# Kernel optimization log

Hardware: AMD Instinct MI355X
Metric: run time of the kernel (lower is better)

The kernel has to match this reference:

```python
import jax, jax.numpy as jnp
import numpy as np


def setup_inputs() -> dict:
    key = jax.random.key(0)
    k1, k2, k3 = jax.random.split(key, 3)
    B, H, S, D = 2, 16, 2048, 64
    return {
        "q": jax.random.normal(k1, (B, H, S, D), dtype=jnp.float32),
        "k": jax.random.normal(k2, (B, H, S, D), dtype=jnp.float32),
        "v": jax.random.normal(k3, (B, H, S, D), dtype=jnp.float32),
        "chunk_size": 256,
    }


def reference(q, k, v, chunk_size):
    # Chunked Based linear attention: linear (K^T V) + rank-3 quadratic (K x K x V)
    # inter-chunk state recurrence (shifted/exclusive cumsum over chunks) plus the
    # intra-chunk causal part with kernel  s = q.k;  phi = s + 0.5*s^2.
    B, H, S, D = q.shape
    C = chunk_size
    N = S // C
    scale = D ** (-0.5)

    qc = (q * scale).reshape(B, H, N, C, D)
    kc = k.reshape(B, H, N, C, D)
    vc = v.reshape(B, H, N, C, D)

    # ---- linear inter-chunk state: shifted cumsum of K^T V per chunk ----
    KV = jnp.einsum("bhncd,bhnce->bhnde", kc, vc)            # (B,H,N,D,D)
    S_lin = jnp.cumsum(KV, axis=2) - KV                       # exclusive cumsum
    o_lin = jnp.einsum("bhncd,bhnde->bhnce", qc, S_lin)

    # ---- quadratic inter-chunk state: shifted cumsum of sum_c K_d K_e V_f ----
    KKV = jnp.einsum("bhncd,bhnce,bhncf->bhndef", kc, kc, vc)  # (B,H,N,D,D,D)
    S_quad = jnp.cumsum(KKV, axis=2) - KKV                     # exclusive cumsum
    o_quad = 0.5 * jnp.einsum("bhndef,bhncd,bhnce->bhncf", S_quad, qc, qc)

    # ---- intra-chunk causal quadratic attention ----
    A = jnp.einsum("bhncd,bhnmd->bhncm", qc, kc)               # (B,H,N,C,C)
    mask = jnp.tril(jnp.ones((C, C), dtype=bool))
    Ak = jnp.where(mask, A + 0.5 * A * A, 0.0)
    o_intra = jnp.einsum("bhncm,bhnmf->bhncf", Ak, vc)

    out = (o_lin + o_quad + o_intra).reshape(B, H, S, D)
    return out
```

## Files before the change

### kernel.cpp

```cpp
#include <hip/hip_runtime.h>
#include <stdint.h>

#define SEQ  2048
#define DH   64
#define BH_N 32
#define SCALE 0.125f

typedef __attribute__((ext_vector_type(8))) short short8;
typedef __attribute__((ext_vector_type(4))) short short4b;
typedef __attribute__((ext_vector_type(4))) float f32x4;

static __device__ __forceinline__ unsigned short f2bf(float f) {
  unsigned int u = __float_as_uint(f);
  u += 0x7fffu + ((u >> 16) & 1u);
  return (unsigned short)(u >> 16);
}

typedef __attribute__((address_space(1))) const unsigned char* gp1;
typedef __attribute__((address_space(3))) unsigned char* lp3;
static __device__ __forceinline__ void stage16(const void* g, void* l) {
  __builtin_amdgcn_global_load_lds((gp1)g, (lp3)l, 16, 0, 0);
}

__global__ __launch_bounds__(256) void prep_kernel(
    const float* __restrict__ kin, const float* __restrict__ vin,
    unsigned short* __restrict__ kb, unsigned short* __restrict__ vt2)
{
  const int sb = blockIdx.x;
  const int bh = blockIdx.y;
  const int t  = threadIdx.x;
  const size_t base = ((size_t)bh * SEQ + (size_t)sb * 64) * DH;

  #pragma unroll
  for (int i = 0; i < 4; ++i) {
    int lin = i * 1024 + t * 4;
    float4 f = *reinterpret_cast<const float4*>(kin + base + lin);
    uint2 pk;
    pk.x = (unsigned)f2bf(f.x) | ((unsigned)f2bf(f.y) << 16);
    pk.y = (unsigned)f2bf(f.z) | ((unsigned)f2bf(f.w) << 16);
    *reinterpret_cast<uint2*>(kb + base + lin) = pk;
  }

  #pragma unroll
  for (int uu = 0; uu < 2; ++uu) {
    const int u   = uu * 256 + t;
    const int kgp = u >> 8, ft = (u >> 6) & 3, qd = (u >> 4) & 3, lo = u & 15;
    unsigned short sh[8];
    #pragma unroll
    for (int j = 0; j < 8; ++j) {
      int kg  = kgp * 2 + (j >> 2);
      int key = kg * 16 + qd * 4 + (j & 3);
      sh[j] = f2bf(vin[base + (size_t)key * DH + ft * 16 + lo]);
    }
    uint4 pk;
    pk.x = (unsigned)sh[0] | ((unsigned)sh[1] << 16);
    pk.y = (unsigned)sh[2] | ((unsigned)sh[3] << 16);
    pk.z = (unsigned)sh[4] | ((unsigned)sh[5] << 16);
    pk.w = (unsigned)sh[6] | ((unsigned)sh[7] << 16);
    *reinterpret_cast<uint4*>(vt2 + (((size_t)bh * 32 + sb) * 512 + u) * 8) = pk;
  }
}

__global__ __launch_bounds__(512, 4) void attn_kernel(
    const float* __restrict__ q,
    const unsigned short* __restrict__ kb,
    const unsigned short* __restrict__ vt2,
    float* __restrict__ out)
{
  const int qa   = blockIdx.x;
  const int bh   = blockIdx.y;
  const int tid  = threadIdx.x;
  const int w    = tid >> 6;
  const int lane = tid & 63;
  const int low  = lane & 15;
  const int quad = lane >> 4;
  const int p    = w >> 2;
  const int qsel = (w >> 1) & 1;
  const int rh   = w & 1;

  const int mytile = qsel ? (31 - qa) : qa;
  const int tmax   = 31 - qa;
  const int imax   = tmax >> 1;
  const int r0     = mytile * 64 + rh * 32;

  __shared__ __align__(16) unsigned short kls[2][2][8][512];
  __shared__ __align__(16) unsigned short vls[2][2][512][8];

  const unsigned short* kb_h = kb  + (size_t)bh * SEQ * DH;
  const unsigned short* v2_h = vt2 + (size_t)bh * 32 * 512 * 8;

  short8 aq[2][2];
  #pragma unroll
  for (int h = 0; h < 2; ++h) {
    const float* qp = q + ((size_t)bh * SEQ + r0 + h * 16 + low) * DH + quad * 8;
    #pragma unroll
    for (int ks = 0; ks < 2; ++ks) {
      float4 f0 = *reinterpret_cast<const float4*>(qp + ks * 32);
      float4 f1 = *reinterpret_cast<const float4*>(qp + ks * 32 + 4);
      short8 a;
      a[0] = (short)f2bf(f0.x * SCALE); a[1] = (short)f2bf(f0.y * SCALE);
      a[2] = (short)f2bf(f0.z * SCALE); a[3] = (short)f2bf(f0.w * SCALE);
      a[4] = (short)f2bf(f1.x * SCALE); a[5] = (short)f2bf(f1.y * SCALE);
      a[6] = (short)f2bf(f1.z * SCALE); a[7] = (short)f2bf(f1.w * SCALE);
      aq[h][ks] = a;
    }
  }

  f32x4 oacc[2][4];
  #pragma unroll
  for (int h = 0; h < 2; ++h)
    #pragma unroll
    for (int i = 0; i < 4; ++i) oacc[h][i] = (f32x4){0.f, 0.f, 0.f, 0.f};

  const int cc = w & 3, pp = w >> 2;

  #define STAGE(IP, B)                                                           \
    do {                                                                         \
      const int tile_ = (IP) * 2 + pp;                                           \
      stage16(kb_h + (size_t)(tile_ * 64 + lane) * 64 + cc * 8,                  \
              &kls[B][pp][cc][0]);                                               \
      stage16(kb_h + (size_t)(tile_ * 64 + lane) * 64 + 32 + cc * 8,             \
              &kls[B][pp][cc + 4][0]);                                           \
      stage16(v2_h + (size_t)(tile_ * 512 + cc * 64 + lane) * 8,                 \
              &vls[B][pp][cc * 64][0]);                                          \
      stage16(v2_h + (size_t)(tile_ * 512 + (cc + 4) * 64 + lane) * 8,           \
              &vls[B][pp][(cc + 4) * 64][0]);                                    \
    } while (0)

  STAGE(0, 0);

  for (int i = 0; i <= imax; ++i) {
    const int b = i & 1;
    __builtin_amdgcn_s_barrier();
    if (i < imax) {
      STAGE(i + 1, b ^ 1);
      asm volatile("s_waitcnt vmcnt(4)" ::: "memory");
    } else {
      asm volatile("s_waitcnt vmcnt(0)" ::: "memory");
    }
    __builtin_amdgcn_s_barrier();
    asm volatile("" ::: "memory");

    const int tt = 2 * i + p;
    if (tt > mytile) continue;
    const bool diag = (tt == mytile);

    const unsigned short* kT = &kls[b][p][0][0];
    const unsigned short* vT = &vls[b][p][0][0];

    #pragma unroll
    for (int ntp = 0; ntp < 2; ++ntp) {
      short8 vf[4];
      #pragma unroll
      for (int ft = 0; ft < 4; ++ft)
        vf[ft] = *reinterpret_cast<const short8*>(
            vT + (ntp * 256 + ft * 64 + quad * 16 + low) * 8);

      #pragma unroll
      for (int sub = 0; sub < 2; ++sub) {
        const int nt = ntp * 2 + sub;

        f32x4 s0 = (f32x4){0.f, 0.f, 0.f, 0.f};
        f32x4 s1 = (f32x4){0.f, 0.f, 0.f, 0.f};
        #pragma unroll
        for (int ks = 0; ks < 2; ++ks) {
          short8 kf = *reinterpret_cast<const short8*>(
              kT + (ks * 4 + quad) * 512 + (nt * 16 + low) * 8);
          s0 = __builtin_amdgcn_mfma_f32_16x16x32_bf16(kf, aq[0][ks], s0, 0, 0, 0);
          s1 = __builtin_amdgcn_mfma_f32_16x16x32_bf16(kf, aq[1][ks], s1, 0, 0, 0);
        }

        #pragma unroll
        for (int h = 0; h < 2; ++h) {
          f32x4 s = h ? s1 : s0;
          short4b pf;
          #pragma unroll
          for (int r = 0; r < 4; ++r) {
            float x = s[r];
            float v = __builtin_fmaf(0.5f * x, x, x);
            if (diag && (nt * 16 + quad * 4 + r) > (rh * 32 + h * 16 + low)) v = 0.f;
            pf[r] = (short)f2bf(v);
          }
          #pragma unroll
          for (int ft = 0; ft < 4; ++ft) {
            short4b va = sub
                ? __builtin_shufflevector(vf[ft], vf[ft], 4, 5, 6, 7)
                : __builtin_shufflevector(vf[ft], vf[ft], 0, 1, 2, 3);
            oacc[h][ft] =
                __builtin_amdgcn_mfma_f32_16x16x16bf16_1k(va, pf, oacc[h][ft], 0, 0, 0);
          }
        }
      }
    }
  }

  __syncthreads();
  float* mb = reinterpret_cast<float*>(&kls[0][0][0][0]);
  float* mw = mb + (size_t)(w & 3) * 2048;
  if (p == 1) {
    #pragma unroll
    for (int h = 0; h < 2; ++h)
      #pragma unroll
      for (int ft = 0; ft < 4; ++ft)
        *reinterpret_cast<f32x4*>(&mw[(h * 4 + ft) * 256 + low * 16 + quad * 4]) =
            oacc[h][ft];
  }
  __syncthreads();
  if (p == 0) {
    #pragma unroll
    for (int h = 0; h < 2; ++h) {
      #pragma unroll
      for (int ft = 0; ft < 4; ++ft) {
        f32x4 o = oacc[h][ft];
        f32x4 m = *reinterpret_cast<const f32x4*>(
            &mw[(h * 4 + ft) * 256 + low * 16 + quad * 4]);
        o += m;
        *reinterpret_cast<f32x4*>(
            &out[((size_t)bh * SEQ + r0 + h * 16 + low) * DH + ft * 16 + quad * 4]) = o;
      }
    }
  }
}

extern "C" void kernel_launch(void* const* d_in, const int* in_sizes, int n_in,
                              void* d_out, int out_size, void* d_ws, size_t ws_size,
                              hipStream_t stream)
{
  const float* q = (const float*)d_in[0];
  const float* k = (const float*)d_in[1];
  const float* v = (const float*)d_in[2];
  float* out = (float*)d_out;

  unsigned short* kb  = (unsigned short*)d_ws;
  unsigned short* vt2 = kb + (size_t)BH_N * SEQ * DH;

  prep_kernel<<<dim3(32, BH_N), 256, 0, stream>>>(k, v, kb, vt2);
  attn_kernel<<<dim3(16, BH_N), 512, 0, stream>>>(q, kb, vt2, out);
}
```

Baseline: 144.8 us.

## Process paired query tiles in one 4-wave block with shared K/V staging

The attention kernel drops from 8 waves to 4 waves per block, and each wave now holds both paired query tiles (qa and 31-qa). The block streams the 33 key tiles needed by the pair only once: even and odd steps split across two wave pairs, with each tile routed to the matching accumulator set. The prep kernel goes through LDS so it can write K in a pre-tiled layout with coalesced loads and stores, and bf16 packing switches to a perm-based helper. The aim is to remove duplicated K/V loads and the lopsided work between the two query tiles. The cost is twice as many accumulator and Q registers per wave and fewer waves per block.

```diff
diff --git a/kernel.cpp b/kernel.cpp
--- a/kernel.cpp
+++ b/kernel.cpp
@@ -15,6 +15,11 @@
   u += 0x7fffu + ((u >> 16) & 1u);
   return (unsigned short)(u >> 16);
 }
+static __device__ __forceinline__ unsigned packbf(float a, float b) {
+  unsigned ua = __float_as_uint(a); ua += 0x7fffu + ((ua >> 16) & 1u);
+  unsigned ub = __float_as_uint(b); ub += 0x7fffu + ((ub >> 16) & 1u);
+  return __builtin_amdgcn_perm(ub, ua, 0x07060302);
+}
 
 typedef __attribute__((address_space(1))) const unsigned char* gp1;
 typedef __attribute__((address_space(3))) unsigned char* lp3;
@@ -24,46 +29,54 @@
 
 __global__ __launch_bounds__(256) void prep_kernel(
     const float* __restrict__ kin, const float* __restrict__ vin,
-    unsigned short* __restrict__ kb, unsigned short* __restrict__ vt2)
+    unsigned short* __restrict__ kb2, unsigned short* __restrict__ vt2)
 {
   const int sb = blockIdx.x;
   const int bh = blockIdx.y;
   const int t  = threadIdx.x;
-  const size_t base = ((size_t)bh * SEQ + (size_t)sb * 64) * DH;
+  __shared__ __align__(16) unsigned short lds[4096];
+  const size_t base  = ((size_t)bh * SEQ + (size_t)sb * 64) * DH;
+  const size_t obase = ((size_t)bh * 32 + sb) * 4096;
 
   #pragma unroll
   for (int i = 0; i < 4; ++i) {
-    int lin = i * 1024 + t * 4;
-    float4 f = *reinterpret_cast<const float4*>(kin + base + lin);
-    uint2 pk;
-    pk.x = (unsigned)f2bf(f.x) | ((unsigned)f2bf(f.y) << 16);
-    pk.y = (unsigned)f2bf(f.z) | ((unsigned)f2bf(f.w) << 16);
-    *reinterpret_cast<uint2*>(kb + base + lin) = pk;
-  }
-
+    int idx = i * 256 + t, key = idx >> 4, F = (idx & 15) * 4;
+    float4 f = *reinterpret_cast<const float4*>(kin + base + key * DH + F);
+    int c = (F >> 5) * 4 + ((F >> 3) & 3), jh = (F >> 2) & 1;
+    uint2 pk; pk.x = packbf(f.x, f.y); pk.y = packbf(f.z, f.w);
+    *reinterpret_cast<uint2*>(lds + (c * 64 + key) * 8 + jh * 4) = pk;
+  }
+  __syncthreads();
   #pragma unroll
   for (int uu = 0; uu < 2; ++uu) {
-    const int u   = uu * 256 + t;
-    const int kgp = u >> 8, ft = (u >> 6) & 3, qd = (u >> 4) & 3, lo = u & 15;
-    unsigned short sh[8];
-    #pragma unroll
-    for (int j = 0; j < 8; ++j) {
-      int kg  = kgp * 2 + (j >> 2);
-      int key = kg * 16 + qd * 4 + (j & 3);
-      sh[j] = f2bf(vin[base + (size_t)key * DH + ft * 16 + lo]);
-    }
-    uint4 pk;
-    pk.x = (unsigned)sh[0] | ((unsigned)sh[1] << 16);
-    pk.y = (unsigned)sh[2] | ((unsigned)sh[3] << 16);
-    pk.z = (unsigned)sh[4] | ((unsigned)sh[5] << 16);
-    pk.w = (unsigned)sh[6] | ((unsigned)sh[7] << 16);
-    *reinterpret_cast<uint4*>(vt2 + (((size_t)bh * 32 + sb) * 512 + u) * 8) = pk;
-  }
-}
-
-__global__ __launch_bounds__(512, 4) void attn_kernel(
+    int u = uu * 256 + t;
+    *reinterpret_cast<uint4*>(kb2 + obase + u * 8) =
+        *reinterpret_cast<const uint4*>(lds + u * 8);
+  }
+  __syncthreads();
+  #pragma unroll
+  for (int i = 0; i < 4; ++i) {
+    int idx = i * 256 + t, key = idx >> 4, F = (idx & 15) * 4;
+    float4 f = *reinterpret_cast<const float4*>(vin + base + key * DH + F);
+    int kgp = key >> 5, qd = (key >> 2) & 3, jj = ((key >> 4) & 1) * 4 + (key & 3);
+    int u0 = kgp * 256 + (F >> 4) * 64 + qd * 16 + (F & 15);
+    lds[(u0 + 0) * 8 + jj] = f2bf(f.x);
+    lds[(u0 + 1) * 8 + jj] = f2bf(f.y);
+    lds[(u0 + 2) * 8 + jj] = f2bf(f.z);
+    lds[(u0 + 3) * 8 + jj] = f2bf(f.w);
+  }
+  __syncthreads();
+  #pragma unroll
+  for (int uu = 0; uu < 2; ++uu) {
+    int u = uu * 256 + t;
+    *reinterpret_cast<uint4*>(vt2 + obase + u * 8) =
+        *reinterpret_cast<const uint4*>(lds + u * 8);
+  }
+}
+
+__global__ __launch_bounds__(256, 2) void attn_kernel(
     const float* __restrict__ q,
-    const unsigned short* __restrict__ kb,
+    const unsigned short* __restrict__ kb2,
     const unsigned short* __restrict__ vt2,
     float* __restrict__ out)
 {
@@ -74,150 +87,170 @@
   const int lane = tid & 63;
   const int low  = lane & 15;
   const int quad = lane >> 4;
-  const int p    = w >> 2;
-  const int qsel = (w >> 1) & 1;
+  const int p    = w >> 1;
   const int rh   = w & 1;
-
-  const int mytile = qsel ? (31 - qa) : qa;
-  const int tmax   = 31 - qa;
-  const int imax   = tmax >> 1;
-  const int r0     = mytile * 64 + rh * 32;
-
-  __shared__ __align__(16) unsigned short kls[2][2][8][512];
-  __shared__ __align__(16) unsigned short vls[2][2][512][8];
-
-  const unsigned short* kb_h = kb  + (size_t)bh * SEQ * DH;
-  const unsigned short* v2_h = vt2 + (size_t)bh * 32 * 512 * 8;
-
-  short8 aq[2][2];
-  #pragma unroll
-  for (int h = 0; h < 2; ++h) {
-    const float* qp = q + ((size_t)bh * SEQ + r0 + h * 16 + low) * DH + quad * 8;
-    #pragma unroll
-    for (int ks = 0; ks < 2; ++ks) {
-      float4 f0 = *reinterpret_cast<const float4*>(qp + ks * 32);
-      float4 f1 = *reinterpret_cast<const float4*>(qp + ks * 32 + 4);
-      short8 a;
-      a[0] = (short)f2bf(f0.x * SCALE); a[1] = (short)f2bf(f0.y * SCALE);
-      a[2] = (short)f2bf(f0.z * SCALE); a[3] = (short)f2bf(f0.w * SCALE);
-      a[4] = (short)f2bf(f1.x * SCALE); a[5] = (short)f2bf(f1.y * SCALE);
-      a[6] = (short)f2bf(f1.z * SCALE); a[7] = (short)f2bf(f1.w * SCALE);
-      aq[h][ks] = a;
-    }
-  }
-
-  f32x4 oacc[2][4];
+  const int nB   = 32 - qa;
+
+  __shared__ __align__(16) unsigned short kls[2][2][4096];
+  __shared__ __align__(16) unsigned short vls[2][2][4096];
+
+  const unsigned short* kb_h = kb2 + (size_t)bh * 32 * 4096;
+  const unsigned short* v2_h = vt2 + (size_t)bh * 32 * 4096;
+
+  short8 aqA[2][2], aqB[2][2];
+  #pragma unroll
+  for (int tsel = 0; tsel < 2; ++tsel) {
+    const int qt = tsel ? (31 - qa) : qa;
+    #pragma unroll
+    for (int h = 0; h < 2; ++h) {
+      const float* qp =
+          q + ((size_t)bh * SEQ + qt * 64 + rh * 32 + h * 16 + low) * DH + quad * 8;
+      #pragma unroll
+      for (int ks = 0; ks < 2; ++ks) {
+        float4 f0 = *reinterpret_cast<const float4*>(qp + ks * 32);
+        float4 f1 = *reinterpret_cast<const float4*>(qp + ks * 32 + 4);
+        uint4 uv;
+        uv.x = packbf(f0.x * SCALE, f0.y * SCALE);
+        uv.y = packbf(f0.z * SCALE, f0.w * SCALE);
+        uv.z = packbf(f1.x * SCALE, f1.y * SCALE);
+        uv.w = packbf(f1.z * SCALE, f1.w * SCALE);
+        short8 a = __builtin_bit_cast(short8, uv);
+        if (tsel) aqB[h][ks] = a; else aqA[h][ks] = a;
+      }
+    }
+  }
+
+  f32x4 oaccA[2][4], oaccB[2][4];
   #pragma unroll
   for (int h = 0; h < 2; ++h)
     #pragma unroll
-    for (int i = 0; i < 4; ++i) oacc[h][i] = (f32x4){0.f, 0.f, 0.f, 0.f};
-
-  const int cc = w & 3, pp = w >> 2;
-
-  #define STAGE(IP, B)                                                           \
-    do {                                                                         \
-      const int tile_ = (IP) * 2 + pp;                                           \
-      stage16(kb_h + (size_t)(tile_ * 64 + lane) * 64 + cc * 8,                  \
-              &kls[B][pp][cc][0]);                                               \
-      stage16(kb_h + (size_t)(tile_ * 64 + lane) * 64 + 32 + cc * 8,             \
-              &kls[B][pp][cc + 4][0]);                                           \
-      stage16(v2_h + (size_t)(tile_ * 512 + cc * 64 + lane) * 8,                 \
-              &vls[B][pp][cc * 64][0]);                                          \
-      stage16(v2_h + (size_t)(tile_ * 512 + (cc + 4) * 64 + lane) * 8,           \
-              &vls[B][pp][(cc + 4) * 64][0]);                                    \
+    for (int i = 0; i < 4; ++i) {
+      oaccA[h][i] = (f32x4){0.f, 0.f, 0.f, 0.f};
+      oaccB[h][i] = (f32x4){0.f, 0.f, 0.f, 0.f};
+    }
+
+  const int slot = w & 1;
+  const unsigned short* gsrc = (w >> 1) ? v2_h : kb_h;
+  unsigned short* ldst0 = (w >> 1) ? &vls[0][slot][0] : &kls[0][slot][0];
+  unsigned short* ldst1 = (w >> 1) ? &vls[1][slot][0] : &kls[1][slot][0];
+
+  #define STAGE(I, B)                                                          \
+    do {                                                                       \
+      int s_ = 2 * (I) + slot; if (s_ > 32) s_ = 32;                           \
+      const int T_ = (s_ < nB) ? s_ : (s_ - nB);                               \
+      const unsigned short* gs_ = gsrc + (size_t)T_ * 4096;                    \
+      unsigned short* ld_ = (B) ? ldst1 : ldst0;                               \
+      _Pragma("unroll")                                                        \
+      for (int r_ = 0; r_ < 8; ++r_)                                           \
+        stage16(gs_ + (r_ * 64 + lane) * 8, ld_ + (r_ * 64 + lane) * 8);       \
     } while (0)
 
+  #define COMPUTE(AQ, OACC)                                                    \
+    do {                                                                       \
+      _Pragma("unroll")                                                        \
+      for (int ntp = 0; ntp < 2; ++ntp) {                                      \
+        short8 vf[4];                                                          \
+        _Pragma("unroll")                                                      \
+        for (int ft = 0; ft < 4; ++ft)                                         \
+          vf[ft] = *reinterpret_cast<const short8*>(                           \
+              vT + ((ntp * 4 + ft) * 64 + quad * 16 + low) * 8);               \
+        _Pragma("unroll")                                                      \
+        for (int sub = 0; sub < 2; ++sub) {                                    \
+          const int nt = ntp * 2 + sub;                                        \
+          f32x4 s0 = (f32x4){0.f, 0.f, 0.f, 0.f};                              \
+          f32x4 s1 = (f32x4){0.f, 0.f, 0.f, 0.f};                              \
+          _Pragma("unroll")                                                    \
+          for (int ks = 0; ks < 2; ++ks) {                                     \
+            short8 kf = *reinterpret_cast<const short8*>(                      \
+                kT + ((ks * 4 + quad) * 64 + nt * 16 + low) * 8);              \
+            s0 = __builtin_amdgcn_mfma_f32_16x16x32_bf16(kf, AQ[0][ks], s0, 0, 0, 0); \
+            s1 = __builtin_amdgcn_mfma_f32_16x16x32_bf16(kf, AQ[1][ks], s1, 0, 0, 0); \
+          }                                                                    \
+          _Pragma("unroll")                                                    \
+          for (int h = 0; h < 2; ++h) {                                        \
+            f32x4 sv = h ? s1 : s0;                                            \
+            float pv[4];                                                       \
+            _Pragma("unroll")                                                  \
+            for (int r = 0; r < 4; ++r) {                                      \
+              float x = sv[r];                                                 \
+              pv[r] = __builtin_fmaf(0.5f * x, x, x);                          \
+            }                                                                  \
+            if (diag) {                                                        \
+              _Pragma("unroll")                                                \
+              for (int r = 0; r < 4; ++r)                                      \
+                if ((nt * 16 + quad * 4 + r) > (rh * 32 + h * 16 + low))       \
+                  pv[r] = 0.f;                                                 \
+            }                                                                  \
+            uint2 du; du.x = packbf(pv[0], pv[1]); du.y = packbf(pv[2], pv[3]);\
+            short4b pf = __builtin_bit_cast(short4b, du);                      \
+            _Pragma("unroll")                                                  \
+            for (int ft = 0; ft < 4; ++ft) {                                   \
+              short4b va = sub                                                 \
+                  ? __builtin_shufflevector(vf[ft], vf[ft], 4, 5, 6, 7)        \
+                  : __builtin_shufflevector(vf[ft], vf[ft], 0, 1, 2, 3);       \
+              OACC[h][ft] = __builtin_amdgcn_mfma_f32_16x16x16bf16_1k(         \
+                  va, pf, OACC[h][ft], 0, 0, 0);                               \
+            }                                                                  \
+          }                                                                    \
+        }                                                                      \
+      }                                                                        \
+    } while (0)
+
   STAGE(0, 0);
 
-  for (int i = 0; i <= imax; ++i) {
+  for (int i = 0; i < 17; ++i) {
     const int b = i & 1;
     __builtin_amdgcn_s_barrier();
-    if (i < imax) {
+    if (i < 16) {
       STAGE(i + 1, b ^ 1);
-      asm volatile("s_waitcnt vmcnt(4)" ::: "memory");
+      asm volatile("s_waitcnt vmcnt(8)" ::: "memory");
     } else {
       asm volatile("s_waitcnt vmcnt(0)" ::: "memory");
     }
     __builtin_amdgcn_s_barrier();
     asm volatile("" ::: "memory");
 
-    const int tt = 2 * i + p;
-    if (tt > mytile) continue;
-    const bool diag = (tt == mytile);
-
-    const unsigned short* kT = &kls[b][p][0][0];
-    const unsigned short* vT = &vls[b][p][0][0];
-
-    #pragma unroll
-    for (int ntp = 0; ntp < 2; ++ntp) {
-      short8 vf[4];
-      #pragma unroll
-      for (int ft = 0; ft < 4; ++ft)
-        vf[ft] = *reinterpret_cast<const short8*>(
-            vT + (ntp * 256 + ft * 64 + quad * 16 + low) * 8);
-
-      #pragma unroll
-      for (int sub = 0; sub < 2; ++sub) {
-        const int nt = ntp * 2 + sub;
-
-        f32x4 s0 = (f32x4){0.f, 0.f, 0.f, 0.f};
-        f32x4 s1 = (f32x4){0.f, 0.f, 0.f, 0.f};
-        #pragma unroll
-        for (int ks = 0; ks < 2; ++ks) {
-          short8 kf = *reinterpret_cast<const short8*>(
-              kT + (ks * 4 + quad) * 512 + (nt * 16 + low) * 8);
-          s0 = __builtin_amdgcn_mfma_f32_16x16x32_bf16(kf, aq[0][ks], s0, 0, 0, 0);
-          s1 = __builtin_amdgcn_mfma_f32_16x16x32_bf16(kf, aq[1][ks], s1, 0, 0, 0);
-        }
-
-        #pragma unroll
-        for (int h = 0; h < 2; ++h) {
-          f32x4 s = h ? s1 : s0;
-          short4b pf;
-          #pragma unroll
-          for (int r = 0; r < 4; ++r) {
-            float x = s[r];
-            float v = __builtin_fmaf(0.5f * x, x, x);
-            if (diag && (nt * 16 + quad * 4 + r) > (rh * 32 + h * 16 + low)) v = 0.f;
-            pf[r] = (short)f2bf(v);
-          }
-          #pragma unroll
-          for (int ft = 0; ft < 4; ++ft) {
-            short4b va = sub
-                ? __builtin_shufflevector(vf[ft], vf[ft], 4, 5, 6, 7)
-                : __builtin_shufflevector(vf[ft], vf[ft], 0, 1, 2, 3);
-            oacc[h][ft] =
-                __builtin_amdgcn_mfma_f32_16x16x16bf16_1k(va, pf, oacc[h][ft], 0, 0, 0);
-          }
-        }
-      }
-    }
-  }
-
-  __syncthreads();
-  float* mb = reinterpret_cast<float*>(&kls[0][0][0][0]);
-  float* mw = mb + (size_t)(w & 3) * 2048;
+    const int s = 2 * i + p;
+    if (s > 32) continue;
+    const bool diag = (s == nB - 1) || (s == 32);
+    const unsigned short* kT = &kls[b][p][0];
+    const unsigned short* vT = &vls[b][p][0];
+
+    if (s >= nB) COMPUTE(aqA, oaccA);
+    else         COMPUTE(aqB, oaccB);
+  }
+
+  __syncthreads();
+  float* mb = reinterpret_cast<float*>(&kls[0][0][0]);
+  float* mw = mb + rh * 4096;
   if (p == 1) {
     #pragma unroll
     for (int h = 0; h < 2; ++h)
       #pragma unroll
-      for (int ft = 0; ft < 4; ++ft)
-        *reinterpret_cast<f32x4*>(&mw[(h * 4 + ft) * 256 + low * 16 + quad * 4]) =
-            oacc[h][ft];
+      for (int ft = 0; ft < 4; ++ft) {
+        *reinterpret_cast<f32x4*>(mw + ((0 * 8 + h * 4 + ft) * 256 + lane * 4)) =
+            oaccA[h][ft];
+        *reinterpret_cast<f32x4*>(mw + ((1 * 8 + h * 4 + ft) * 256 + lane * 4)) =
+            oaccB[h][ft];
+      }
   }
   __syncthreads();
   if (p == 0) {
     #pragma unroll
-    for (int h = 0; h < 2; ++h) {
+    for (int tsel = 0; tsel < 2; ++tsel) {
+      const int qt = tsel ? (31 - qa) : qa;
       #pragma unroll
-      for (int ft = 0; ft < 4; ++ft) {
-        f32x4 o = oacc[h][ft];
-        f32x4 m = *reinterpret_cast<const f32x4*>(
-            &mw[(h * 4 + ft) * 256 + low * 16 + quad * 4]);
-        o += m;
-        *reinterpret_cast<f32x4*>(
-            &out[((size_t)bh * SEQ + r0 + h * 16 + low) * DH + ft * 16 + quad * 4]) = o;
-      }
+      for (int h = 0; h < 2; ++h)
+        #pragma unroll
+        for (int ft = 0; ft < 4; ++ft) {
+          f32x4 o = tsel ? oaccB[h][ft] : oaccA[h][ft];
+          f32x4 m = *reinterpret_cast<const f32x4*>(
+              mw + ((tsel * 8 + h * 4 + ft) * 256 + lane * 4));
+          o += m;
+          *reinterpret_cast<f32x4*>(
+              out + ((size_t)bh * SEQ + qt * 64 + rh * 32 + h * 16 + low) * DH +
+              ft * 16 + quad * 4) = o;
+        }
     }
   }
 }
@@ -231,9 +264,9 @@
   const float* v = (const float*)d_in[2];
   float* out = (float*)d_out;
 
-  unsigned short* kb  = (unsigned short*)d_ws;
-  unsigned short* vt2 = kb + (size_t)BH_N * SEQ * DH;
-
-  prep_kernel<<<dim3(32, BH_N), 256, 0, stream>>>(k, v, kb, vt2);
-  attn_kernel<<<dim3(16, BH_N), 512, 0, stream>>>(q, kb, vt2, out);
-}
+  unsigned short* kb2 = (unsigned short*)d_ws;
+  unsigned short* vt2 = kb2 + (size_t)BH_N * SEQ * DH;
+
+  prep_kernel<<<dim3(32, BH_N), 256, 0, stream>>>(k, v, kb2, vt2);
+  attn_kernel<<<dim3(16, BH_N), 256, 0, stream>>>(q, kb2, vt2, out);
+}
```

After: 128.2 us. 11.5% less time.

## Restructure attention into 256-thread blocks with LDS-transposed prep and swizzled grid

Applied to the files above, without the earlier changes.

The prep kernel now transposes K and V through shared memory into the exact per-tile fragment layouts, so loads are coalesced and the LDS staging in the attention kernel becomes contiguous 16-byte copies. The attention kernel drops from 512 to 256 threads per block. Each block now walks every key tile sequentially instead of splitting tiles across two wave groups, which removes the final cross-wave LDS reduction. The grid is flattened with a block-to-head swizzle, and bf16 packing uses a perm-based helper. This trades parallel work per block for higher occupancy and fewer barriers, at the cost of a longer serial loop per block.

```diff
diff --git a/kernel.cpp b/kernel.cpp
--- a/kernel.cpp
+++ b/kernel.cpp
@@ -15,6 +15,11 @@
   u += 0x7fffu + ((u >> 16) & 1u);
   return (unsigned short)(u >> 16);
 }
+static __device__ __forceinline__ unsigned packbf(float a, float b) {
+  unsigned ua = __float_as_uint(a); ua += 0x7fffu + ((ua >> 16) & 1u);
+  unsigned ub = __float_as_uint(b); ub += 0x7fffu + ((ub >> 16) & 1u);
+  return __builtin_amdgcn_perm(ub, ua, 0x07060302);
+}
 
 typedef __attribute__((address_space(1))) const unsigned char* gp1;
 typedef __attribute__((address_space(3))) unsigned char* lp3;
@@ -24,85 +29,91 @@
 
 __global__ __launch_bounds__(256) void prep_kernel(
     const float* __restrict__ kin, const float* __restrict__ vin,
-    unsigned short* __restrict__ kb, unsigned short* __restrict__ vt2)
+    unsigned short* __restrict__ kb2, unsigned short* __restrict__ vt2)
 {
   const int sb = blockIdx.x;
   const int bh = blockIdx.y;
   const int t  = threadIdx.x;
-  const size_t base = ((size_t)bh * SEQ + (size_t)sb * 64) * DH;
+  __shared__ __align__(16) unsigned short lds[4096];
+  const size_t base  = ((size_t)bh * SEQ + (size_t)sb * 64) * DH;
+  const size_t obase = ((size_t)bh * 32 + sb) * 4096;
 
   #pragma unroll
   for (int i = 0; i < 4; ++i) {
-    int lin = i * 1024 + t * 4;
-    float4 f = *reinterpret_cast<const float4*>(kin + base + lin);
-    uint2 pk;
-    pk.x = (unsigned)f2bf(f.x) | ((unsigned)f2bf(f.y) << 16);
-    pk.y = (unsigned)f2bf(f.z) | ((unsigned)f2bf(f.w) << 16);
-    *reinterpret_cast<uint2*>(kb + base + lin) = pk;
-  }
-
+    int idx = i * 256 + t, key = idx >> 4, F = (idx & 15) * 4;
+    float4 f = *reinterpret_cast<const float4*>(kin + base + key * DH + F);
+    int c = (F >> 5) * 4 + ((F >> 3) & 3), jh = (F >> 2) & 1;
+    uint2 pk; pk.x = packbf(f.x, f.y); pk.y = packbf(f.z, f.w);
+    *reinterpret_cast<uint2*>(lds + (c * 64 + key) * 8 + jh * 4) = pk;
+  }
+  __syncthreads();
   #pragma unroll
   for (int uu = 0; uu < 2; ++uu) {
-    const int u   = uu * 256 + t;
-    const int kgp = u >> 8, ft = (u >> 6) & 3, qd = (u >> 4) & 3, lo = u & 15;
-    unsigned short sh[8];
-    #pragma unroll
-    for (int j = 0; j < 8; ++j) {
-      int kg  = kgp * 2 + (j >> 2);
-      int key = kg * 16 + qd * 4 + (j & 3);
-      sh[j] = f2bf(vin[base + (size_t)key * DH + ft * 16 + lo]);
-    }
-    uint4 pk;
-    pk.x = (unsigned)sh[0] | ((unsigned)sh[1] << 16);
-    pk.y = (unsigned)sh[2] | ((unsigned)sh[3] << 16);
-    pk.z = (unsigned)sh[4] | ((unsigned)sh[5] << 16);
-    pk.w = (unsigned)sh[6] | ((unsigned)sh[7] << 16);
-    *reinterpret_cast<uint4*>(vt2 + (((size_t)bh * 32 + sb) * 512 + u) * 8) = pk;
-  }
-}
-
-__global__ __launch_bounds__(512, 4) void attn_kernel(
+    int u = uu * 256 + t;
+    *reinterpret_cast<uint4*>(kb2 + obase + u * 8) =
+        *reinterpret_cast<const uint4*>(lds + u * 8);
+  }
+  __syncthreads();
+  #pragma unroll
+  for (int i = 0; i < 4; ++i) {
+    int idx = i * 256 + t, key = idx >> 4, F = (idx & 15) * 4;
+    float4 f = *reinterpret_cast<const float4*>(vin + base + key * DH + F);
+    int kgp = key >> 5, qd = (key >> 2) & 3, jj = ((key >> 4) & 1) * 4 + (key & 3);
+    int u0 = kgp * 256 + (F >> 4) * 64 + qd * 16 + (F & 15);
+    lds[(u0 + 0) * 8 + jj] = f2bf(f.x);
+    lds[(u0 + 1) * 8 + jj] = f2bf(f.y);
+    lds[(u0 + 2) * 8 + jj] = f2bf(f.z);
+    lds[(u0 + 3) * 8 + jj] = f2bf(f.w);
+  }
+  __syncthreads();
+  #pragma unroll
+  for (int uu = 0; uu < 2; ++uu) {
+    int u = uu * 256 + t;
+    *reinterpret_cast<uint4*>(vt2 + obase + u * 8) =
+        *reinterpret_cast<const uint4*>(lds + u * 8);
+  }
+}
+
+__global__ __launch_bounds__(256, 5) void attn_kernel(
     const float* __restrict__ q,
-    const unsigned short* __restrict__ kb,
+    const unsigned short* __restrict__ kb2,
     const unsigned short* __restrict__ vt2,
     float* __restrict__ out)
 {
-  const int qa   = blockIdx.x;
-  const int bh   = blockIdx.y;
+  const int b0   = blockIdx.x;
+  const int bh   = (b0 & 7) | (((b0 >> 3) & 3) << 3);
+  const int qa   = b0 >> 5;
   const int tid  = threadIdx.x;
   const int w    = tid >> 6;
   const int lane = tid & 63;
   const int low  = lane & 15;
   const int quad = lane >> 4;
-  const int p    = w >> 2;
-  const int qsel = (w >> 1) & 1;
   const int rh   = w & 1;
 
-  const int mytile = qsel ? (31 - qa) : qa;
-  const int tmax   = 31 - qa;
-  const int imax   = tmax >> 1;
+  const int mytile = (w < 2) ? (31 - qa) : qa;
+  const int nIter  = 32 - qa;
   const int r0     = mytile * 64 + rh * 32;
 
-  __shared__ __align__(16) unsigned short kls[2][2][8][512];
-  __shared__ __align__(16) unsigned short vls[2][2][512][8];
-
-  const unsigned short* kb_h = kb  + (size_t)bh * SEQ * DH;
-  const unsigned short* v2_h = vt2 + (size_t)bh * 32 * 512 * 8;
+  __shared__ __align__(16) unsigned short buf[2][8192];
+
+  const unsigned short* kb_h = kb2 + (size_t)bh * 32 * 4096;
+  const unsigned short* v2_h = vt2 + (size_t)bh * 32 * 4096;
 
   short8 aq[2][2];
   #pragma unroll
   for (int h = 0; h < 2; ++h) {
-    const float* qp = q + ((size_t)bh * SEQ + r0 + h * 16 + low) * DH + quad * 8;
+    const float* qp =
+        q + ((size_t)bh * SEQ + r0 + h * 16 + low) * DH + quad * 8;
     #pragma unroll
     for (int ks = 0; ks < 2; ++ks) {
       float4 f0 = *reinterpret_cast<const float4*>(qp + ks * 32);
       float4 f1 = *reinterpret_cast<const float4*>(qp + ks * 32 + 4);
-      short8 a;
-      a[0] = (short)f2bf(f0.x * SCALE); a[1] = (short)f2bf(f0.y * SCALE);
-      a[2] = (short)f2bf(f0.z * SCALE); a[3] = (short)f2bf(f0.w * SCALE);
-      a[4] = (short)f2bf(f1.x * SCALE); a[5] = (short)f2bf(f1.y * SCALE);
-      a[6] = (short)f2bf(f1.z * SCALE); a[7] = (short)f2bf(f1.w * SCALE);
-      aq[h][ks] = a;
+      uint4 uv;
+      uv.x = packbf(f0.x * SCALE, f0.y * SCALE);
+      uv.y = packbf(f0.z * SCALE, f0.w * SCALE);
+      uv.z = packbf(f1.x * SCALE, f1.y * SCALE);
+      uv.w = packbf(f1.z * SCALE, f1.w * SCALE);
+      aq[h][ks] = __builtin_bit_cast(short8, uv);
     }
   }
 
@@ -112,28 +123,25 @@
     #pragma unroll
     for (int i = 0; i < 4; ++i) oacc[h][i] = (f32x4){0.f, 0.f, 0.f, 0.f};
 
-  const int cc = w & 3, pp = w >> 2;
-
-  #define STAGE(IP, B)                                                           \
-    do {                                                                         \
-      const int tile_ = (IP) * 2 + pp;                                           \
-      stage16(kb_h + (size_t)(tile_ * 64 + lane) * 64 + cc * 8,                  \
-              &kls[B][pp][cc][0]);                                               \
-      stage16(kb_h + (size_t)(tile_ * 64 + lane) * 64 + 32 + cc * 8,             \
-              &kls[B][pp][cc + 4][0]);                                           \
-      stage16(v2_h + (size_t)(tile_ * 512 + cc * 64 + lane) * 8,                 \
-              &vls[B][pp][cc * 64][0]);                                          \
-      stage16(v2_h + (size_t)(tile_ * 512 + (cc + 4) * 64 + lane) * 8,           \
-              &vls[B][pp][(cc + 4) * 64][0]);                                    \
+  const unsigned short* gsrc = (w < 2) ? kb_h : v2_h;
+  const int ghalf = (w & 1) * 2048;
+
+  #define STAGE(T, B)                                                          \
+    do {                                                                       \
+      const unsigned short* gs_ = gsrc + (size_t)(T) * 4096 + ghalf;           \
+      unsigned short* ld_ = &buf[B][w * 2048];                                 \
+      _Pragma("unroll")                                                        \
+      for (int r_ = 0; r_ < 4; ++r_)                                           \
+        stage16(gs_ + r_ * 512 + lane * 8, ld_ + r_ * 512 + lane * 8);         \
     } while (0)
 
   STAGE(0, 0);
 
-  for (int i = 0; i <= imax; ++i) {
-    const int b = i & 1;
+  for (int t = 0; t < nIter; ++t) {
+    const int bb = t & 1;
     __builtin_amdgcn_s_barrier();
-    if (i < imax) {
-      STAGE(i + 1, b ^ 1);
+    if (t < nIter - 1) {
+      STAGE(t + 1, bb ^ 1);
       asm volatile("s_waitcnt vmcnt(4)" ::: "memory");
     } else {
       asm volatile("s_waitcnt vmcnt(0)" ::: "memory");
@@ -141,12 +149,10 @@
     __builtin_amdgcn_s_barrier();
     asm volatile("" ::: "memory");
 
-    const int tt = 2 * i + p;
-    if (tt > mytile) continue;
-    const bool diag = (tt == mytile);
-
-    const unsigned short* kT = &kls[b][p][0][0];
-    const unsigned short* vT = &vls[b][p][0][0];
+    if (t > mytile) continue;
+    const bool diag = (t == mytile);
+    const unsigned short* kT = &buf[bb][0];
+    const unsigned short* vT = &buf[bb][4096];
 
     #pragma unroll
     for (int ntp = 0; ntp < 2; ++ntp) {
@@ -154,72 +160,56 @@
       #pragma unroll
       for (int ft = 0; ft < 4; ++ft)
         vf[ft] = *reinterpret_cast<const short8*>(
-            vT + (ntp * 256 + ft * 64 + quad * 16 + low) * 8);
+            vT + ((ntp * 4 + ft) * 64 + quad * 16 + low) * 8);
 
       #pragma unroll
       for (int sub = 0; sub < 2; ++sub) {
         const int nt = ntp * 2 + sub;
-
         f32x4 s0 = (f32x4){0.f, 0.f, 0.f, 0.f};
         f32x4 s1 = (f32x4){0.f, 0.f, 0.f, 0.f};
         #pragma unroll
         for (int ks = 0; ks < 2; ++ks) {
           short8 kf = *reinterpret_cast<const short8*>(
-              kT + (ks * 4 + quad) * 512 + (nt * 16 + low) * 8);
+              kT + ((ks * 4 + quad) * 64 + nt * 16 + low) * 8);
           s0 = __builtin_amdgcn_mfma_f32_16x16x32_bf16(kf, aq[0][ks], s0, 0, 0, 0);
           s1 = __builtin_amdgcn_mfma_f32_16x16x32_bf16(kf, aq[1][ks], s1, 0, 0, 0);
         }
-
         #pragma unroll
         for (int h = 0; h < 2; ++h) {
-          f32x4 s = h ? s1 : s0;
-          short4b pf;
+          f32x4 sv = h ? s1 : s0;
+          float pv[4];
           #pragma unroll
           for (int r = 0; r < 4; ++r) {
-            float x = s[r];
-            float v = __builtin_fmaf(0.5f * x, x, x);
-            if (diag && (nt * 16 + quad * 4 + r) > (rh * 32 + h * 16 + low)) v = 0.f;
-            pf[r] = (short)f2bf(v);
+            float x = sv[r];
+            pv[r] = __builtin_fmaf(0.5f * x, x, x);
           }
+          if (diag) {
+            #pragma unroll
+            for (int r = 0; r < 4; ++r)
+              if ((nt * 16 + quad * 4 + r) > (rh * 32 + h * 16 + low)) pv[r] = 0.f;
+          }
+          uint2 du; du.x = packbf(pv[0], pv[1]); du.y = packbf(pv[2], pv[3]);
+          short4b pf = __builtin_bit_cast(short4b, du);
           #pragma unroll
           for (int ft = 0; ft < 4; ++ft) {
             short4b va = sub
                 ? __builtin_shufflevector(vf[ft], vf[ft], 4, 5, 6, 7)
                 : __builtin_shufflevector(vf[ft], vf[ft], 0, 1, 2, 3);
-            oacc[h][ft] =
-                __builtin_amdgcn_mfma_f32_16x16x16bf16_1k(va, pf, oacc[h][ft], 0, 0, 0);
+            oacc[h][ft] = __builtin_amdgcn_mfma_f32_16x16x16bf16_1k(
+                va, pf, oacc[h][ft], 0, 0, 0);
           }
         }
       }
     }
   }
 
-  __syncthreads();
-  float* mb = reinterpret_cast<float*>(&kls[0][0][0][0]);
-  float* mw = mb + (size_t)(w & 3) * 2048;
-  if (p == 1) {
-    #pragma unroll
-    for (int h = 0; h < 2; ++h)
-      #pragma unroll
-      for (int ft = 0; ft < 4; ++ft)
-        *reinterpret_cast<f32x4*>(&mw[(h * 4 + ft) * 256 + low * 16 + quad * 4]) =
-            oacc[h][ft];
-  }
-  __syncthreads();
-  if (p == 0) {
-    #pragma unroll
-    for (int h = 0; h < 2; ++h) {
-      #pragma unroll
-      for (int ft = 0; ft < 4; ++ft) {
-        f32x4 o = oacc[h][ft];
-        f32x4 m = *reinterpret_cast<const f32x4*>(
-            &mw[(h * 4 + ft) * 256 + low * 16 + quad * 4]);
-        o += m;
-        *reinterpret_cast<f32x4*>(
-            &out[((size_t)bh * SEQ + r0 + h * 16 + low) * DH + ft * 16 + quad * 4]) = o;
-      }
-    }
-  }
+  #pragma unroll
+  for (int h = 0; h < 2; ++h)
+    #pragma unroll
+    for (int ft = 0; ft < 4; ++ft)
+      *reinterpret_cast<f32x4*>(
+          out + ((size_t)bh * SEQ + r0 + h * 16 + low) * DH + ft * 16 + quad * 4) =
+          oacc[h][ft];
 }
 
 extern "C" void kernel_launch(void* const* d_in, const int* in_sizes, int n_in,
@@ -231,9 +221,9 @@
   const float* v = (const float*)d_in[2];
   float* out = (float*)d_out;
 
-  unsigned short* kb  = (unsigned short*)d_ws;
-  unsigned short* vt2 = kb + (size_t)BH_N * SEQ * DH;
-
-  prep_kernel<<<dim3(32, BH_N), 256, 0, stream>>>(k, v, kb, vt2);
-  attn_kernel<<<dim3(16, BH_N), 512, 0, stream>>>(q, kb, vt2, out);
-}
+  unsigned short* kb2 = (unsigned short*)d_ws;
+  unsigned short* vt2 = kb2 + (size_t)BH_N * SEQ * DH;
+
+  prep_kernel<<<dim3(32, BH_N), 256, 0, stream>>>(k, v, kb2, vt2);
+  attn_kernel<<<512, 256, 0, stream>>>(q, kb2, vt2, out);
+}
```

New measurement: 153.3 us. 1.06x slower.
